# Performance work log

Measured on AMD Instinct MI355X. Metric: run time of the kernel, lower is better.

## Reference

```python
import jax, jax.numpy as jnp
import numpy as np

B, S, D = 4, 2048, 1024


def setup_inputs() -> dict:
    key = jax.random.key(0)
    ks = jax.random.split(key, 7)
    s = 1.0 / np.sqrt(D)
    return {
        "x": jax.random.normal(ks[0], (B, S, D), dtype=jnp.float32),
        "Wq": jax.random.normal(ks[1], (D, D), dtype=jnp.float32) * s,
        "bq": jnp.zeros((D,), dtype=jnp.float32),
        "Wk": jax.random.normal(ks[2], (D, D), dtype=jnp.float32) * s,
        "bk": jnp.zeros((D,), dtype=jnp.float32),
        "Wv": jax.random.normal(ks[3], (D, D), dtype=jnp.float32) * s,
        "bv": jnp.zeros((D,), dtype=jnp.float32),
    }


def reference(x, Wq, bq, Wk, bk, Wv, bv):
    # Linear layers: x @ W^T + b (torch nn.Linear convention)
    Q = jnp.einsum("bsd,ed->bse", x, Wq) + bq
    K = jnp.einsum("bsd,ed->bse", x, Wk) + bk
    V = jnp.einsum("bsd,ed->bse", x, Wv) + bv
    scale = 1.0 / (x.shape[-1] ** 0.5)
    scores = jnp.einsum("bse,bte->bst", Q, K) * scale  # [B, S, S]
    attn = jax.nn.softmax(scores, axis=-1)
    out = jnp.einsum("bst,bte->bse", attn, V)
    return out
```

## Files before the change

kernel.cpp:

```cpp
#include <hip/hip_runtime.h>
#include <math.h>


typedef _Float16 f16;
typedef _Float16 f16x8 __attribute__((ext_vector_type(8)));
typedef _Float16 f16x4 __attribute__((ext_vector_type(4)));
typedef float f32x4 __attribute__((ext_vector_type(4)));

__device__ __forceinline__ void glds16(const void* g, const void* l) {
    __builtin_amdgcn_global_load_lds(
        (const __attribute__((address_space(1))) void*)g,
        (__attribute__((address_space(3))) void*)l, 16, 0, 0);
}

#define VMCNT(n)  asm volatile("s_waitcnt vmcnt(" #n ")" ::: "memory")
#define LGKM(n)   asm volatile("s_waitcnt lgkmcnt(" #n ")" ::: "memory")
#define BARRIER() asm volatile("s_barrier" ::: "memory")
#define SCHEDB()  __builtin_amdgcn_sched_barrier(0)

__global__ __launch_bounds__(256) void prep_kernel(
    const float* __restrict__ x,
    const float* __restrict__ Wq, const float* __restrict__ Wk,
    const float* __restrict__ Wv,
    f16* __restrict__ xh, f16* __restrict__ Wh3, float* __restrict__ sums)
{
    const int bid = blockIdx.x, tid = threadIdx.x;
    if (bid < 8) {
        float4 z = {0.f, 0.f, 0.f, 0.f};
        ((float4*)sums)[bid * 256 + tid] = z;
    }
    if (bid < 8192) {
        const int i = bid * 256 + tid;
        float4 v = ((const float4*)x)[i];
        f16x4 h = { (f16)v.x, (f16)v.y, (f16)v.z, (f16)v.w };
        ((f16x4*)xh)[i] = h;
    } else {
        const int wid   = bid - 8192;
        const int plane = wid >> 10;
        const int i     = (wid & 1023) * 256 + tid;
        const float* src = (plane == 0) ? Wq : (plane == 1) ? Wk : Wv;
        float4 v = ((const float4*)src)[i];
        f16x4 h = { (f16)v.x, (f16)v.y, (f16)v.z, (f16)v.w };
        ((f16x4*)(Wh3 + (size_t)plane * 1024 * 1024))[i] = h;
    }
}

#define ABUF 16384
#define BBUF 8192
#define BOFF 49152

__device__ __forceinline__ void mfma_core3(
    const f16* A, int lda,
    const f16* B, int ldb,
    int K, int m0, int n0, f16* sm, f32x4 acc[4][4])
{
    const int tid  = threadIdx.x;
    const int lane = tid & 63;
    const int w    = tid >> 6;
    const int wr   = w >> 1;
    const int wc   = w & 1;
    const int lr   = lane & 15;
    const int kq   = lane >> 4;

    const int rl = lane >> 3;
    const int ch = (lane & 7) ^ rl;

    const f16* gA[4];
    #pragma unroll
    for (int p = 0; p < 4; ++p)
        gA[p] = A + (size_t)(m0 + p * 64 + w * 8 + rl) * lda + ch * 8;
    const f16* gB[2];
    #pragma unroll
    for (int p = 0; p < 2; ++p)
        gB[p] = B + (size_t)(n0 + p * 64 + w * 8 + rl) * ldb + ch * 8;

    const int NT = K >> 6;

    f16* sA0 = sm;             f16* sB0 = sm + BOFF;
    f16* sA1 = sm + ABUF;      f16* sB1 = sm + BOFF + BBUF;
    f16* sA2 = sm + 2 * ABUF;  f16* sB2 = sm + BOFF + 2 * BBUF;

    #define STAGE(kofs, dA, dB) do {                                          \
        _Pragma("unroll")                                                     \
        for (int p = 0; p < 4; ++p)                                           \
            glds16(gA[p] + (kofs), (dA) + w * 512 + p * 4096);                \
        _Pragma("unroll")                                                     \
        for (int p = 0; p < 2; ++p)                                           \
            glds16(gB[p] + (kofs), (dB) + w * 512 + p * 4096);                \
    } while (0)

    STAGE(0,  sA0, sB0);
    STAGE(64, sA1, sB1);

    int kst = 128;
    f16* curA = sA0; f16* curB = sB0;
    f16* nxtA = sA1; f16* nxtB = sB1;
    f16* farA = sA2; f16* farB = sB2;

    for (int t = 0; t < NT; ++t) {
        if (t + 2 < NT) {
            STAGE(kst, farA, farB);
            kst += 64;
            VMCNT(12);
        } else if (t + 1 < NT) {
            VMCNT(6);
        } else {
            VMCNT(0);
        }
        BARRIER();

        {
            f16x8 a[4], b[4];
            #pragma unroll
            for (int i = 0; i < 4; ++i) {
                const int ra = wr * 64 + i * 16 + lr;
                a[i] = *(const f16x8*)&curA[ra * 64 + ((kq ^ (ra & 7)) * 8)];
            }
            #pragma unroll
            for (int j = 0; j < 4; ++j) {
                const int rb = wc * 64 + j * 16 + lr;
                b[j] = *(const f16x8*)&curB[rb * 64 + ((kq ^ (rb & 7)) * 8)];
            }
            LGKM(0);
            SCHEDB();
            __builtin_amdgcn_s_setprio(1);
            #pragma unroll
            for (int i = 0; i < 4; ++i)
                #pragma unroll
                for (int j = 0; j < 4; ++j)
                    acc[i][j] = __builtin_amdgcn_mfma_f32_16x16x32_f16(a[i], b[j], acc[i][j], 0, 0, 0);
            __builtin_amdgcn_s_setprio(0);
        }
        {
            f16x8 a[4], b[4];
            const int c = 4 + kq;
            #pragma unroll
            for (int i = 0; i < 4; ++i) {
                const int ra = wr * 64 + i * 16 + lr;
                a[i] = *(const f16x8*)&curA[ra * 64 + ((c ^ (ra & 7)) * 8)];
            }
            #pragma unroll
            for (int j = 0; j < 4; ++j) {
                const int rb = wc * 64 + j * 16 + lr;
                b[j] = *(const f16x8*)&curB[rb * 64 + ((c ^ (rb & 7)) * 8)];
            }
            LGKM(0);
            BARRIER();
            SCHEDB();
            __builtin_amdgcn_s_setprio(1);
            #pragma unroll
            for (int i = 0; i < 4; ++i)
                #pragma unroll
                for (int j = 0; j < 4; ++j)
                    acc[i][j] = __builtin_amdgcn_mfma_f32_16x16x32_f16(a[i], b[j], acc[i][j], 0, 0, 0);
            __builtin_amdgcn_s_setprio(0);
        }

        f16* tA = curA; f16* tB = curB;
        curA = nxtA; curB = nxtB;
        nxtA = farA; nxtB = farB;
        farA = tA;   farB = tB;
    }
    #undef STAGE
}

__device__ __forceinline__ void mfma_core8w(
    const f16* A, int lda,
    const f16* B, int ldb,
    int K, int m0, int n0, f16* sm, f32x4 (&acc)[8][4])
{
    const int tid  = threadIdx.x;
    const int lane = tid & 63;
    const int w    = tid >> 6;
    const int wr   = w >> 2;
    const int wn   = w & 3;
    const int lr   = lane & 15;
    const int kq   = lane >> 4;

    const int rl = lane >> 3;
    const int ch = (lane & 7) ^ rl;

    const f16* gA[4];
    #pragma unroll
    for (int p = 0; p < 4; ++p)
        gA[p] = A + (size_t)(m0 + p * 64 + w * 8 + rl) * lda + ch * 8;
    const f16* gB[4];
    #pragma unroll
    for (int p = 0; p < 4; ++p)
        gB[p] = B + (size_t)(n0 + p * 64 + w * 8 + rl) * ldb + ch * 8;

    const int NT = K >> 6;

    f16* sA0 = sm;              f16* sA1 = sm + 16384;
    f16* sB0 = sm + 32768;      f16* sB1 = sm + 49152;

    #define STAGE8(kofs, dA, dB) do {                                         \
        _Pragma("unroll")                                                     \
        for (int p = 0; p < 4; ++p)                                           \
            glds16(gA[p] + (kofs), (dA) + w * 512 + p * 4096);                \
        _Pragma("unroll")                                                     \
        for (int p = 0; p < 4; ++p)                                           \
            glds16(gB[p] + (kofs), (dB) + w * 512 + p * 4096);                \
    } while (0)

    STAGE8(0, sA0, sB0);

    f16* curA = sA0; f16* curB = sB0;
    f16* othA = sA1; f16* othB = sB1;

    for (int t = 0; t < NT; ++t) {
        if (t + 1 < NT) {
            STAGE8((t + 1) * 64, othA, othB);
            VMCNT(8);
        } else {
            VMCNT(0);
        }
        BARRIER();

        #pragma unroll
        for (int kk = 0; kk < 2; ++kk) {
            f16x8 a[8], b[4];
            const int c = kk * 4 + kq;
            #pragma unroll
            for (int i = 0; i < 8; ++i) {
                const int ra = wr * 128 + i * 16 + lr;
                a[i] = *(const f16x8*)&curA[ra * 64 + ((c ^ (ra & 7)) * 8)];
            }
            #pragma unroll
            for (int j = 0; j < 4; ++j) {
                const int rb = wn * 64 + j * 16 + lr;
                b[j] = *(const f16x8*)&curB[rb * 64 + ((c ^ (rb & 7)) * 8)];
            }
            LGKM(0);
            if (kk == 1) BARRIER();
            SCHEDB();
            __builtin_amdgcn_s_setprio(1);
            #pragma unroll
            for (int i = 0; i < 8; ++i)
                #pragma unroll
                for (int j = 0; j < 4; ++j)
                    acc[i][j] = __builtin_amdgcn_mfma_f32_16x16x32_f16(a[i], b[j], acc[i][j], 0, 0, 0);
            __builtin_amdgcn_s_setprio(0);
        }

        f16* x;
        x = curA; curA = othA; othA = x;
        x = curB; curB = othB; othB = x;
    }
    #undef STAGE8
}

__global__ __launch_bounds__(512) void qkv_mfma_kernel(
    const f16* __restrict__ xh, const f16* __restrict__ Wh,
    const float* __restrict__ bq, const float* __restrict__ bk,
    const float* __restrict__ bv,
    f16* __restrict__ Qh, f16* __restrict__ Kh, f16* __restrict__ Vt)
{
    extern __shared__ __align__(16) f16 smem[];
    int flat = blockIdx.x + 8 * (blockIdx.y + 32 * blockIdx.z);
    flat = (flat & 7) * 96 + (flat >> 3);
    const int bx = flat & 7;
    const int by = (flat >> 3) & 31;
    const int bz = flat >> 8;

    const int m0 = by * 256;
    const int n0 = bx * 128;

    f32x4 acc[4][4];
    #pragma unroll
    for (int i = 0; i < 4; ++i)
        #pragma unroll
        for (int j = 0; j < 4; ++j) acc[i][j] = (f32x4){0.f, 0.f, 0.f, 0.f};

    mfma_core3(xh, 1024, Wh + (size_t)bz * 1024 * 1024, 1024, 1024, m0, n0, smem, acc);

    const int lane = threadIdx.x & 63;
    const int w    = threadIdx.x >> 6;
    const int wm = (w >> 1) * 64;
    const int wn = (w & 1) * 64;
    const int col  = lane & 15;
    const int quad = lane >> 4;

    if (bz == 2) {
        #pragma unroll
        for (int i = 0; i < 4; ++i) {
            const int gmb = m0 + wm + i * 16 + quad * 4;
            const int bb_ = gmb >> 11;
            const int s   = gmb & 2047;
            f16* vtb = Vt + (size_t)bb_ * 1024 * 2048;
            #pragma unroll
            for (int j = 0; j < 4; ++j) {
                const int gn = n0 + wn + j * 16 + col;
                const float bbv = bv[gn];
                f16x4 v = { (f16)(acc[i][j][0] + bbv), (f16)(acc[i][j][1] + bbv),
                            (f16)(acc[i][j][2] + bbv), (f16)(acc[i][j][3] + bbv) };
                *(f16x4*)&vtb[(size_t)gn * 2048 + s] = v;
            }
        }
    } else {
        const float* bias = (bz == 0) ? bq : bk;
        const float  sc   = (bz == 0) ? 0.03125f : 1.0f;
        f16* C = (bz == 0) ? Qh : Kh;
        #pragma unroll
        for (int j = 0; j < 4; ++j) {
            const int gn = n0 + wn + j * 16 + col;
            const float bb = bias[gn];
            #pragma unroll
            for (int i = 0; i < 4; ++i)
                #pragma unroll
                for (int r = 0; r < 4; ++r) {
                    const int gm = m0 + wm + i * 16 + quad * 4 + r;
                    C[(size_t)gm * 1024 + gn] = (f16)((acc[i][j][r] + bb) * sc);
                }
        }
    }
}

__global__ __launch_bounds__(512, 2) void scores_exp_kernel(
    const f16* __restrict__ Qh, const f16* __restrict__ Kh,
    f16* __restrict__ P, float* __restrict__ sums)
{
    extern __shared__ __align__(16) f16 smem[];
    const int b  = blockIdx.z;
    const int m0 = blockIdx.y * 256;
    const int n0 = blockIdx.x * 256;

    f32x4 acc[8][4];
    #pragma unroll
    for (int i = 0; i < 8; ++i)
        #pragma unroll
        for (int j = 0; j < 4; ++j) acc[i][j] = (f32x4){0.f, 0.f, 0.f, 0.f};

    const size_t ao = (size_t)b * 2048 * 1024;
    mfma_core8w(Qh + ao, 1024, Kh + ao, 1024, 1024, m0, n0, smem, acc);

    const int lane = threadIdx.x & 63;
    const int w    = threadIdx.x >> 6;
    const int wr = w >> 2, wn = w & 3;
    const int col  = lane & 15;
    const int quad = lane >> 4;
    f16* C = P + (size_t)b * 2048 * 2048;

    float rp[8][4];
    #pragma unroll
    for (int i = 0; i < 8; ++i)
        #pragma unroll
        for (int r = 0; r < 4; ++r) rp[i][r] = 0.0f;

    #pragma unroll
    for (int i = 0; i < 8; ++i)
        #pragma unroll
        for (int r = 0; r < 4; ++r) {
            const int gm = m0 + wr * 128 + i * 16 + quad * 4 + r;
            #pragma unroll
            for (int j = 0; j < 4; ++j) {
                const int gn = n0 + wn * 64 + j * 16 + col;
                const f16 p = (f16)__expf(acc[i][j][r]);
                C[(size_t)gm * 2048 + gn] = p;
                rp[i][r] += (float)p;
            }
        }

    #pragma unroll
    for (int i = 0; i < 8; ++i)
        #pragma unroll
        for (int r = 0; r < 4; ++r) {
            float v = rp[i][r];
            v += __shfl_xor(v, 1);
            v += __shfl_xor(v, 2);
            v += __shfl_xor(v, 4);
            v += __shfl_xor(v, 8);
            rp[i][r] = v;
        }
    if (col == 0) {
        #pragma unroll
        for (int i = 0; i < 8; ++i)
            #pragma unroll
            for (int r = 0; r < 4; ++r) {
                const int row = m0 + wr * 128 + i * 16 + quad * 4 + r;
                atomicAdd(&sums[b * 2048 + row], rp[i][r]);
            }
    }
}

__global__ __launch_bounds__(512) void pv_mfma_kernel(
    const f16* __restrict__ P, const f16* __restrict__ Vt,
    const float* __restrict__ sums, float* __restrict__ out)
{
    extern __shared__ __align__(16) f16 smem[];
    const int b  = blockIdx.z;
    const int m0 = blockIdx.y * 256;
    const int n0 = blockIdx.x * 128;

    f32x4 acc[4][4];
    #pragma unroll
    for (int i = 0; i < 4; ++i)
        #pragma unroll
        for (int j = 0; j < 4; ++j) acc[i][j] = (f32x4){0.f, 0.f, 0.f, 0.f};

    const size_t ao = (size_t)b * 2048 * 2048;
    const size_t bo = (size_t)b * 1024 * 2048;
    mfma_core3(P + ao, 2048, Vt + bo, 2048, 2048, m0, n0, smem, acc);

    const int lane = threadIdx.x & 63;
    const int w    = threadIdx.x >> 6;
    const int wm = (w >> 1) * 64;
    const int wn = (w & 1) * 64;
    const int col  = lane & 15;
    const int quad = lane >> 4;
    float* C = out + (size_t)b * 2048 * 1024;

    #pragma unroll
    for (int i = 0; i < 4; ++i)
        #pragma unroll
        for (int r = 0; r < 4; ++r) {
            const int rl = m0 + wm + i * 16 + quad * 4 + r;
            const float inv = 1.0f / sums[b * 2048 + rl];
            #pragma unroll
            for (int j = 0; j < 4; ++j) {
                const int gn = n0 + wn + j * 16 + col;
                C[(size_t)rl * 1024 + gn] = acc[i][j][r] * inv;
            }
        }
}

extern "C" void kernel_launch(void* const* d_in, const int* in_sizes, int n_in,
                              void* d_out, int out_size, void* d_ws, size_t ws_size,
                              hipStream_t stream)
{
    (void)in_sizes; (void)n_in; (void)out_size; (void)ws_size;
    const int Bn = 4, S = 2048, D = 1024;
    const float* x  = (const float*)d_in[0];
    const float* Wq = (const float*)d_in[1];
    const float* bq = (const float*)d_in[2];
    const float* Wk = (const float*)d_in[3];
    const float* bk = (const float*)d_in[4];
    const float* Wv = (const float*)d_in[5];
    const float* bv = (const float*)d_in[6];
    float* out = (float*)d_out;

    const size_t MB = 1024 * 1024;
    char* w = (char*)d_ws;
    f16*   xh   = (f16*)(w + 0 * MB);
    f16*   Wh3  = (f16*)(w + 16 * MB);
    f16*   Qh   = (f16*)(w + 38 * MB);
    f16*   Kh   = (f16*)(w + 54 * MB);
    f16*   Vt   = (f16*)(w + 70 * MB);
    float* sums = (float*)(w + 86 * MB);
    f16*   P    = (f16*)(w + 0 * MB);

    static bool attr_set = false;
    if (!attr_set) {
        (void)hipFuncSetAttribute(reinterpret_cast<const void*>(qkv_mfma_kernel),
                            hipFuncAttributeMaxDynamicSharedMemorySize, 147456);
        (void)hipFuncSetAttribute(reinterpret_cast<const void*>(scores_exp_kernel),
                            hipFuncAttributeMaxDynamicSharedMemorySize, 131072);
        (void)hipFuncSetAttribute(reinterpret_cast<const void*>(pv_mfma_kernel),
                            hipFuncAttributeMaxDynamicSharedMemorySize, 147456);
        attr_set = true;
    }

    prep_kernel<<<dim3(11264), 256, 0, stream>>>(x, Wq, Wk, Wv, xh, Wh3, sums);

    qkv_mfma_kernel<<<dim3(D / 128, (Bn * S) / 256, 3), 512, 147456, stream>>>(
        xh, Wh3, bq, bk, bv, Qh, Kh, Vt);

    scores_exp_kernel<<<dim3(S / 256, S / 256, Bn), 512, 131072, stream>>>(
        Qh, Kh, P, sums);
    pv_mfma_kernel<<<dim3(D / 128, S / 256, Bn), 512, 147456, stream>>>(
        P, Vt, sums, out);
}
```

Measured before the change: 247.4 us.

## Fuse Q, K, V projections into one kernel sharing each x tile

Replaces the three-plane QKV GEMM launch with a single kernel in which each block computes matching 256x128 tiles of Q, K and V. The staged x tile is loaded into LDS once and reused against three weight tiles, which cuts repeated global reads of x. In exchange each thread holds three accumulator sets, raising register pressure, and the grid shrinks from 768 to 256 blocks, which may leave compute units underused. The launch bound of 2 blocks per CU also conflicts with the 160KB of LDS each block requests.

```diff
diff --git a/kernel.cpp b/kernel.cpp
--- a/kernel.cpp
+++ b/kernel.cpp
@@ -45,6 +45,147 @@
     }
 }
 
+__global__ __launch_bounds__(512, 2) void qkv_fused_kernel(
+    const f16* __restrict__ xh, const f16* __restrict__ Wh3,
+    const float* __restrict__ bq, const float* __restrict__ bk,
+    const float* __restrict__ bv,
+    f16* __restrict__ Qh, f16* __restrict__ Kh, f16* __restrict__ Vt)
+{
+    extern __shared__ __align__(16) f16 smem[];
+    const int bx = blockIdx.x >> 5;
+    const int by = blockIdx.x & 31;
+    const int m0 = by * 256;
+    const int n0 = bx * 128;
+
+    const int tid  = threadIdx.x;
+    const int lane = tid & 63;
+    const int w    = tid >> 6;
+    const int wr   = w >> 1;
+    const int wc   = w & 1;
+    const int lr   = lane & 15;
+    const int kq   = lane >> 4;
+
+    const int rl = lane >> 3;
+    const int ch = (lane & 7) ^ rl;
+
+    unsigned oA[4];
+    #pragma unroll
+    for (int p = 0; p < 4; ++p)
+        oA[p] = (unsigned)((m0 + p * 64 + w * 8 + rl) * 1024 + ch * 8);
+    unsigned oB[6];
+    #pragma unroll
+    for (int p = 0; p < 6; ++p) {
+        const int g  = w * 48 + p * 8;
+        const int pl = g >> 7;
+        const int rp = g & 127;
+        oB[p] = (unsigned)(pl * 1048576 + (n0 + rp + rl) * 1024 + ch * 8);
+    }
+
+    f16* sA0 = smem;                f16* sA1 = smem + 16384;
+    f16* sB0 = smem + 32768;        f16* sB1 = smem + 32768 + 24576;
+
+    #define STAGEF(kofs, dA, dB) do {                                         \
+        _Pragma("unroll")                                                     \
+        for (int p = 0; p < 4; ++p)                                           \
+            glds16(xh + oA[p] + (kofs), (dA) + w * 512 + p * 4096);           \
+        _Pragma("unroll")                                                     \
+        for (int p = 0; p < 6; ++p)                                           \
+            glds16(Wh3 + oB[p] + (kofs), (dB) + w * 3072 + p * 512);          \
+    } while (0)
+
+    f32x4 aQ[4][4], aK[4][4], aV[4][4];
+    #pragma unroll
+    for (int i = 0; i < 4; ++i)
+        #pragma unroll
+        for (int j = 0; j < 4; ++j) {
+            aQ[i][j] = (f32x4){0.f, 0.f, 0.f, 0.f};
+            aK[i][j] = (f32x4){0.f, 0.f, 0.f, 0.f};
+            aV[i][j] = (f32x4){0.f, 0.f, 0.f, 0.f};
+        }
+
+    STAGEF(0, sA0, sB0);
+    f16* curA = sA0; f16* curB = sB0;
+    f16* othA = sA1; f16* othB = sB1;
+
+    for (int t = 0; t < 16; ++t) {
+        if (t < 15) { STAGEF((t + 1) * 64, othA, othB); VMCNT(10); }
+        else        { VMCNT(0); }
+        BARRIER();
+
+        #pragma unroll
+        for (int kk = 0; kk < 2; ++kk) {
+            const int c = kk * 4 + kq;
+            f16x8 a[4];
+            #pragma unroll
+            for (int i = 0; i < 4; ++i) {
+                const int ra = wr * 64 + i * 16 + lr;
+                a[i] = *(const f16x8*)&curA[ra * 64 + ((c ^ (ra & 7)) * 8)];
+            }
+            #define ZBLOCK(zi, ACC, ISLAST) do {                              \
+                f16x8 b[4];                                                   \
+                _Pragma("unroll")                                             \
+                for (int j = 0; j < 4; ++j) {                                 \
+                    const int rb = (zi) * 128 + wc * 64 + j * 16 + lr;        \
+                    b[j] = *(const f16x8*)&curB[rb * 64 + ((c ^ (rb & 7)) * 8)]; \
+                }                                                             \
+                LGKM(0);                                                      \
+                if (ISLAST) BARRIER();          \
+                SCHEDB();                                                     \
+                __builtin_amdgcn_s_setprio(1);                                \
+                _Pragma("unroll")                                             \
+                for (int i = 0; i < 4; ++i)                                   \
+                    _Pragma("unroll")                                         \
+                    for (int j = 0; j < 4; ++j)                               \
+                        ACC[i][j] = __builtin_amdgcn_mfma_f32_16x16x32_f16(   \
+                            a[i], b[j], ACC[i][j], 0, 0, 0);                  \
+                __builtin_amdgcn_s_setprio(0);                                \
+            } while (0)
+
+            ZBLOCK(0, aQ, false);
+            ZBLOCK(1, aK, false);
+            ZBLOCK(2, aV, kk == 1);
+            #undef ZBLOCK
+        }
+
+        f16* xp;
+        xp = curA; curA = othA; othA = xp;
+        xp = curB; curB = othB; othB = xp;
+    }
+    #undef STAGEF
+
+    const int col  = lr;
+    const int quad = kq;
+    #pragma unroll
+    for (int j = 0; j < 4; ++j) {
+        const int gn = n0 + wc * 64 + j * 16 + col;
+        const float bbq = bq[gn];
+        const float bbk = bk[gn];
+        #pragma unroll
+        for (int i = 0; i < 4; ++i)
+            #pragma unroll
+            for (int r = 0; r < 4; ++r) {
+                const int gm = m0 + wr * 64 + i * 16 + quad * 4 + r;
+                Qh[(size_t)gm * 1024 + gn] = (f16)((aQ[i][j][r] + bbq) * 0.03125f);
+                Kh[(size_t)gm * 1024 + gn] = (f16)(aK[i][j][r] + bbk);
+            }
+    }
+    #pragma unroll
+    for (int i = 0; i < 4; ++i) {
+        const int gmb = m0 + wr * 64 + i * 16 + quad * 4;
+        const int bb_ = gmb >> 11;
+        const int s   = gmb & 2047;
+        f16* vtb = Vt + (size_t)bb_ * 1024 * 2048;
+        #pragma unroll
+        for (int j = 0; j < 4; ++j) {
+            const int gn = n0 + wc * 64 + j * 16 + col;
+            const float bbv = bv[gn];
+            f16x4 v = { (f16)(aV[i][j][0] + bbv), (f16)(aV[i][j][1] + bbv),
+                        (f16)(aV[i][j][2] + bbv), (f16)(aV[i][j][3] + bbv) };
+            *(f16x4*)&vtb[(size_t)gn * 2048 + s] = v;
+        }
+    }
+}
+
 #define ABUF 16384
 #define BBUF 8192
 #define BOFF 49152
@@ -248,72 +389,6 @@
         x = curB; curB = othB; othB = x;
     }
     #undef STAGE8
-}
-
-__global__ __launch_bounds__(512) void qkv_mfma_kernel(
-    const f16* __restrict__ xh, const f16* __restrict__ Wh,
-    const float* __restrict__ bq, const float* __restrict__ bk,
-    const float* __restrict__ bv,
-    f16* __restrict__ Qh, f16* __restrict__ Kh, f16* __restrict__ Vt)
-{
-    extern __shared__ __align__(16) f16 smem[];
-    int flat = blockIdx.x + 8 * (blockIdx.y + 32 * blockIdx.z);
-    flat = (flat & 7) * 96 + (flat >> 3);
-    const int bx = flat & 7;
-    const int by = (flat >> 3) & 31;
-    const int bz = flat >> 8;
-
-    const int m0 = by * 256;
-    const int n0 = bx * 128;
-
-    f32x4 acc[4][4];
-    #pragma unroll
-    for (int i = 0; i < 4; ++i)
-        #pragma unroll
-        for (int j = 0; j < 4; ++j) acc[i][j] = (f32x4){0.f, 0.f, 0.f, 0.f};
-
-    mfma_core3(xh, 1024, Wh + (size_t)bz * 1024 * 1024, 1024, 1024, m0, n0, smem, acc);
-
-    const int lane = threadIdx.x & 63;
-    const int w    = threadIdx.x >> 6;
-    const int wm = (w >> 1) * 64;
-    const int wn = (w & 1) * 64;
-    const int col  = lane & 15;
-    const int quad = lane >> 4;
-
-    if (bz == 2) {
-        #pragma unroll
-        for (int i = 0; i < 4; ++i) {
-            const int gmb = m0 + wm + i * 16 + quad * 4;
-            const int bb_ = gmb >> 11;
-            const int s   = gmb & 2047;
-            f16* vtb = Vt + (size_t)bb_ * 1024 * 2048;
-            #pragma unroll
-            for (int j = 0; j < 4; ++j) {
-                const int gn = n0 + wn + j * 16 + col;
-                const float bbv = bv[gn];
-                f16x4 v = { (f16)(acc[i][j][0] + bbv), (f16)(acc[i][j][1] + bbv),
-                            (f16)(acc[i][j][2] + bbv), (f16)(acc[i][j][3] + bbv) };
-                *(f16x4*)&vtb[(size_t)gn * 2048 + s] = v;
-            }
-        }
-    } else {
-        const float* bias = (bz == 0) ? bq : bk;
-        const float  sc   = (bz == 0) ? 0.03125f : 1.0f;
-        f16* C = (bz == 0) ? Qh : Kh;
-        #pragma unroll
-        for (int j = 0; j < 4; ++j) {
-            const int gn = n0 + wn + j * 16 + col;
-            const float bb = bias[gn];
-            #pragma unroll
-            for (int i = 0; i < 4; ++i)
-                #pragma unroll
-                for (int r = 0; r < 4; ++r) {
-                    const int gm = m0 + wm + i * 16 + quad * 4 + r;
-                    C[(size_t)gm * 1024 + gn] = (f16)((acc[i][j][r] + bb) * sc);
-                }
-        }
-    }
 }
 
 __global__ __launch_bounds__(512, 2) void scores_exp_kernel(
@@ -451,8 +526,8 @@
 
     static bool attr_set = false;
     if (!attr_set) {
-        (void)hipFuncSetAttribute(reinterpret_cast<const void*>(qkv_mfma_kernel),
-                            hipFuncAttributeMaxDynamicSharedMemorySize, 147456);
+        (void)hipFuncSetAttribute(reinterpret_cast<const void*>(qkv_fused_kernel),
+                            hipFuncAttributeMaxDynamicSharedMemorySize, 163840);
         (void)hipFuncSetAttribute(reinterpret_cast<const void*>(scores_exp_kernel),
                             hipFuncAttributeMaxDynamicSharedMemorySize, 131072);
         (void)hipFuncSetAttribute(reinterpret_cast<const void*>(pv_mfma_kernel),
@@ -462,7 +537,7 @@
 
     prep_kernel<<<dim3(11264), 256, 0, stream>>>(x, Wq, Wk, Wv, xh, Wh3, sums);
 
-    qkv_mfma_kernel<<<dim3(D / 128, (Bn * S) / 256, 3), 512, 147456, stream>>>(
+    qkv_fused_kernel<<<dim3(256), 512, 163840, stream>>>(
         xh, Wh3, bq, bk, bv, Qh, Kh, Vt);
 
     scores_exp_kernel<<<dim3(S / 256, S / 256, Bn), 512, 131072, stream>>>(
```

Result: no change. 245.7 us (-0.7%).
